# Performance work log

Hardware: AMD Instinct MI355X
Metric: run time of the kernel (lower is better)

## Reference

```python
import jax, jax.numpy as jnp
import numpy as np

N_TOKENS = 16384
IN_FEATURES = 1024
OUT_FEATURES = 1024
BH = 32  # block rows (out dim)
BW = 32  # block cols (in dim)
N_BLOCKS = 256  # density 0.25 * (1024*1024/(32*32))


def setup_inputs() -> dict:
    key = jax.random.key(0)
    k1, k2, k3, k4 = jax.random.split(key, 4)
    x = jax.random.normal(k1, (N_TOKENS, IN_FEATURES), dtype=jnp.float32)
    weight_data = jax.random.normal(k2, (N_BLOCKS, BH, BW), dtype=jnp.float32)
    bias = jnp.zeros((OUT_FEATURES,), dtype=jnp.float32)
    block_row = jax.random.randint(k3, (N_BLOCKS,), 0, OUT_FEATURES // BH, dtype=jnp.int32)
    block_col = jax.random.randint(k4, (N_BLOCKS,), 0, IN_FEATURES // BW, dtype=jnp.int32)
    return {"x": x, "weight_data": weight_data, "bias": bias,
            "block_row": block_row, "block_col": block_col}


def reference(x, weight_data, bias, block_row, block_col):
    # Block-sparse linear: y = x @ W^T + bias, with W[out, in] stored as
    # N_BLOCKS dense (BH, BW) blocks at (block_row, block_col) block coords.
    N = x.shape[0]
    B, bh, bw = weight_data.shape
    n_row_blocks = bias.shape[0] // bh
    x3 = x.reshape(N, -1, bw)           # [N, in/bw, bw]
    xb = x3[:, block_col, :]            # gather input block-columns: [N, B, bw]
    # per-block partial output rows: data[b] @ x_colblock -> [N, B, bh]
    partial = jnp.einsum('nbw,bow->nbo', xb, weight_data)
    y3 = jnp.zeros((N, n_row_blocks, bh), dtype=x.dtype).at[:, block_row, :].add(partial)
    return y3.reshape(N, -1) + bias
```

## Files before the change

kernel.cpp:

```cpp
#include <hip/hip_runtime.h>

#define N_TOKENS 16384
#define IN_F 1024
#define OUT_F 1024
#define NB 256
#define BH 32
#define BW 32
#define NRB 32
#define T_TILE 32
#define XS_STRIDE 1040
#define MAX_SCHED (NB + NRB)
#define SCHED_PAD (MAX_SCHED + 2)
#define WF_SLOT_SHORTS 1024

#define WS_WF_BYTES   (SCHED_PAD * WF_SLOT_SHORTS * 2)
#define WS_SCHED_OFF  WS_WF_BYTES
#define WS_POS_OFF    (WS_SCHED_OFF + SCHED_PAD * 4)
#define WS_WSTART_OFF (WS_POS_OFF + NB * 4)

typedef short short8 __attribute__((ext_vector_type(8)));
typedef float float4v __attribute__((ext_vector_type(4)));

__device__ __forceinline__ short f2bf(float f) {
    unsigned u = __builtin_bit_cast(unsigned, f);
    u += 0x7fffu + ((u >> 16) & 1u);
    return (short)(u >> 16);
}

__global__ void prep_sched_kernel(const int* __restrict__ brow, const int* __restrict__ bcol,
                                  int* __restrict__ sched, int* __restrict__ pos_of,
                                  int* __restrict__ wstart, short* __restrict__ wf)
{
    __shared__ int cnt[NRB], start[NRB], cur[NRB];
    const int tid = threadIdx.x;
    if (tid < NRB) { cnt[tid] = 0; cur[tid] = 0; }
    __syncthreads();
    const int r = brow[tid];
    const int c = bcol[tid];
    atomicAdd(&cnt[r], 1);
    __syncthreads();
    if (tid < NRB) {
        const int w = tid & 3, i = tid >> 2;
        int s = 0;
        for (int rr = 0; rr < NRB; ++rr) {
            const int adj = cnt[rr] > 0 ? cnt[rr] : 1;
            const int ww = rr & 3, ii = rr >> 2;
            if (ww < w || (ww == w && ii < i)) s += adj;
        }
        start[tid] = s;
    }
    if (tid >= 64 && tid < 69) {
        const int w = tid - 64;
        int s = 0;
        for (int rr = 0; rr < NRB; ++rr) {
            const int adj = cnt[rr] > 0 ? cnt[rr] : 1;
            if ((rr & 3) < w) s += adj;
        }
        wstart[w] = s;
    }
    __syncthreads();
    const int slot = atomicAdd(&cur[r], 1);
    const int pos = start[r] + slot;
    sched[pos] = c | (r << 5) | ((slot == cnt[r] - 1) ? (1 << 10) : 0);
    pos_of[tid] = pos;
    if (tid < NRB && cnt[tid] == 0) {
        sched[start[tid]] = (tid << 5) | (1 << 10);
        int4 z = {0, 0, 0, 0};
        int4* dst = (int4*)(wf + (size_t)start[tid] * WF_SLOT_SHORTS);
        for (int q = 0; q < WF_SLOT_SHORTS / 8; ++q) dst[q] = z;
    }
}

__global__ void prep_w_kernel(const float* __restrict__ wd, const int* __restrict__ pos_of,
                              short* __restrict__ wf)
{
    const int g = blockIdx.x * blockDim.x + threadIdx.x;
    const int lane = g & 63;
    const int oh = (g >> 6) & 1;
    const int b = g >> 7;
    const int l16 = lane & 15, quad = lane >> 4;
    const int pos = pos_of[b];
    const float* src = wd + (size_t)b * (BH * BW) + (oh * 16 + l16) * BW + quad * 8;
    const float4 w0 = *(const float4*)src;
    const float4 w1 = *(const float4*)(src + 4);
    short8 o;
    o[0] = f2bf(w0.x); o[1] = f2bf(w0.y); o[2] = f2bf(w0.z); o[3] = f2bf(w0.w);
    o[4] = f2bf(w1.x); o[5] = f2bf(w1.y); o[6] = f2bf(w1.z); o[7] = f2bf(w1.w);
    *(short8*)(wf + (size_t)pos * WF_SLOT_SHORTS + oh * 512 + lane * 8) = o;
}

__global__ __launch_bounds__(256, 2) void spmm_main_kernel(
    const float* __restrict__ x, const float* __restrict__ bias,
    const short* __restrict__ wf, const int* __restrict__ sched_g,
    const int* __restrict__ wstart_g, float* __restrict__ out)
{
    __shared__ short xs[T_TILE * XS_STRIDE];
    __shared__ int ssched[SCHED_PAD];
    __shared__ int swstart[5];

    const int tid = threadIdx.x;
    const int n0 = blockIdx.x * T_TILE;

    {
        const int tr = tid >> 7;
        const int tc = tid & 127;
        const float* xp = x + (size_t)(n0 + tr) * IN_F + tc * 8;
        short* sp = xs + tr * XS_STRIDE + tc * 8;
#pragma unroll
        for (int it = 0; it < T_TILE / 2; ++it) {
            const float4 a = *(const float4*)xp;
            const float4 b = *(const float4*)(xp + 4);
            short8 s;
            s[0] = f2bf(a.x); s[1] = f2bf(a.y); s[2] = f2bf(a.z); s[3] = f2bf(a.w);
            s[4] = f2bf(b.x); s[5] = f2bf(b.y); s[6] = f2bf(b.z); s[7] = f2bf(b.w);
            *(short8*)sp = s;
            xp += 2 * IN_F;
            sp += 2 * XS_STRIDE;
        }
    }
    ssched[tid] = sched_g[tid];
    if (tid < SCHED_PAD - 256) ssched[256 + tid] = sched_g[256 + tid];
    if (tid < 5) swstart[tid] = wstart_g[tid];
    __syncthreads();

    const int lane = tid & 63;
    const int wave = tid >> 6;
    const int l16 = lane & 15, quad = lane >> 4;

    const int s = swstart[wave];
    const int e = swstart[wave + 1];

    const short* x0 = xs + l16 * XS_STRIDE + quad * 8;
    const short* x1 = xs + (16 + l16) * XS_STRIDE + quad * 8;
    const short* wfl = wf + lane * 8;

    int e0 = ssched[s];
    int e1 = ssched[s + 1];
    short8 a0_0 = *(const short8*)(x0 + (e0 & 31) * BW);
    short8 a0_1 = *(const short8*)(x1 + (e0 & 31) * BW);
    short8 wA0 = *(const short8*)(wfl + (size_t)s * WF_SLOT_SHORTS);
    short8 wB0 = *(const short8*)(wfl + (size_t)s * WF_SLOT_SHORTS + 512);
    short8 wA1 = *(const short8*)(wfl + (size_t)(s + 1) * WF_SLOT_SHORTS);
    short8 wB1 = *(const short8*)(wfl + (size_t)(s + 1) * WF_SLOT_SHORTS + 512);

    int rn = wave;
    float bv0 = bias[rn * BH + l16];
    float bv1 = bias[rn * BH + 16 + l16];

    float4v acc00 = {0.f, 0.f, 0.f, 0.f};
    float4v acc01 = {0.f, 0.f, 0.f, 0.f};
    float4v acc10 = {0.f, 0.f, 0.f, 0.f};
    float4v acc11 = {0.f, 0.f, 0.f, 0.f};

    for (int k = s; k < e; ++k) {
        const int ep = ssched[k + 2];
        const short8 wA2 = *(const short8*)(wfl + (size_t)(k + 2) * WF_SLOT_SHORTS);
        const short8 wB2 = *(const short8*)(wfl + (size_t)(k + 2) * WF_SLOT_SHORTS + 512);
        const short8 a1_0 = *(const short8*)(x0 + (e1 & 31) * BW);
        const short8 a1_1 = *(const short8*)(x1 + (e1 & 31) * BW);

        acc00 = __builtin_amdgcn_mfma_f32_16x16x32_bf16(a0_0, wA0, acc00, 0, 0, 0);
        acc01 = __builtin_amdgcn_mfma_f32_16x16x32_bf16(a0_0, wB0, acc01, 0, 0, 0);
        acc10 = __builtin_amdgcn_mfma_f32_16x16x32_bf16(a0_1, wA0, acc10, 0, 0, 0);
        acc11 = __builtin_amdgcn_mfma_f32_16x16x32_bf16(a0_1, wB0, acc11, 0, 0, 0);

        if (e0 & (1 << 10)) {
            const int r = (e0 >> 5) & 31;
            const int ob = r * BH + l16;
            float* op0 = out + (size_t)(n0 + quad * 4) * OUT_F + ob;
            float* op1 = out + (size_t)(n0 + 16 + quad * 4) * OUT_F + ob;
#pragma unroll
            for (int g = 0; g < 4; ++g) {
                op0[g * OUT_F]      = acc00[g] + bv0;
                op0[g * OUT_F + 16] = acc01[g] + bv1;
                op1[g * OUT_F]      = acc10[g] + bv0;
                op1[g * OUT_F + 16] = acc11[g] + bv1;
            }
            acc00 = (float4v){0.f, 0.f, 0.f, 0.f};
            acc01 = (float4v){0.f, 0.f, 0.f, 0.f};
            acc10 = (float4v){0.f, 0.f, 0.f, 0.f};
            acc11 = (float4v){0.f, 0.f, 0.f, 0.f};
            rn = (rn + 4) & 31;
            bv0 = bias[rn * BH + l16];
            bv1 = bias[rn * BH + 16 + l16];
        }
        e0 = e1; e1 = ep;
        a0_0 = a1_0; a0_1 = a1_1;
        wA0 = wA1; wB0 = wB1;
        wA1 = wA2; wB1 = wB2;
    }
}

extern "C" void kernel_launch(void* const* d_in, const int* in_sizes, int n_in,
                              void* d_out, int out_size, void* d_ws, size_t ws_size,
                              hipStream_t stream) {
    const float* x    = (const float*)d_in[0];
    const float* wd   = (const float*)d_in[1];
    const float* bias = (const float*)d_in[2];
    const int* brow   = (const int*)d_in[3];
    const int* bcol   = (const int*)d_in[4];
    float* out = (float*)d_out;

    char* ws = (char*)d_ws;
    short* wf   = (short*)ws;
    int* sched  = (int*)(ws + WS_SCHED_OFF);
    int* pos_of = (int*)(ws + WS_POS_OFF);
    int* wstart = (int*)(ws + WS_WSTART_OFF);

    prep_sched_kernel<<<1, 256, 0, stream>>>(brow, bcol, sched, pos_of, wstart, wf);
    prep_w_kernel<<<NB * 128 / 256, 256, 0, stream>>>(wd, pos_of, wf);
    spmm_main_kernel<<<N_TOKENS / T_TILE, 256, 0, stream>>>(x, bias, wf, sched, wstart, out);
}
```

Measured before the change: 137.4 us.

## Split output row-blocks across eight waves and unroll schedule loop by two

Doubles the block to 512 threads so eight waves each own a quarter as many output row-blocks, and pads each wave's schedule to an even length. The main loop is unrolled by two with weight prefetch four slots ahead and two x-tile fragments loaded per iteration. The aim is shorter per-wave serial chains and more memory-level parallelism on the weight loads. The cost is more registers per thread under a tighter launch bound, plus padding entries with zero weights that may read uninitialized weight slots.

```diff
diff --git a/kernel.cpp b/kernel.cpp
--- a/kernel.cpp
+++ b/kernel.cpp
@@ -8,14 +8,15 @@
 #define BW 32
 #define NRB 32
 #define T_TILE 32
+#define NW 8
 #define XS_STRIDE 1040
-#define MAX_SCHED (NB + NRB)
-#define SCHED_PAD (MAX_SCHED + 2)
+#define SCHED_ALLOC 304
 #define WF_SLOT_SHORTS 1024
-
-#define WS_WF_BYTES   (SCHED_PAD * WF_SLOT_SHORTS * 2)
+#define FLUSH_BIT (1 << 10)
+
+#define WS_WF_BYTES   (SCHED_ALLOC * WF_SLOT_SHORTS * 2)
 #define WS_SCHED_OFF  WS_WF_BYTES
-#define WS_POS_OFF    (WS_SCHED_OFF + SCHED_PAD * 4)
+#define WS_POS_OFF    (WS_SCHED_OFF + SCHED_ALLOC * 4)
 #define WS_WSTART_OFF (WS_POS_OFF + NB * 4)
 
 typedef short short8 __attribute__((ext_vector_type(8)));
@@ -40,31 +41,54 @@
     atomicAdd(&cnt[r], 1);
     __syncthreads();
     if (tid < NRB) {
-        const int w = tid & 3, i = tid >> 2;
+        const int w = tid & 7;
         int s = 0;
-        for (int rr = 0; rr < NRB; ++rr) {
-            const int adj = cnt[rr] > 0 ? cnt[rr] : 1;
-            const int ww = rr & 3, ii = rr >> 2;
-            if (ww < w || (ww == w && ii < i)) s += adj;
-        }
+        for (int w2 = 0; w2 < w; ++w2) {
+            int t = 0;
+            for (int rr = w2; rr < NRB; rr += NW) t += (cnt[rr] ? cnt[rr] : 1);
+            s += (t + 1) & ~1;
+        }
+        for (int rr = w; rr < tid; rr += NW) s += (cnt[rr] ? cnt[rr] : 1);
         start[tid] = s;
     }
-    if (tid >= 64 && tid < 69) {
+    if (tid >= 64 && tid < 64 + NW + 1) {
         const int w = tid - 64;
         int s = 0;
-        for (int rr = 0; rr < NRB; ++rr) {
-            const int adj = cnt[rr] > 0 ? cnt[rr] : 1;
-            if ((rr & 3) < w) s += adj;
+        for (int w2 = 0; w2 < w; ++w2) {
+            int t = 0;
+            for (int rr = w2; rr < NRB; rr += NW) t += (cnt[rr] ? cnt[rr] : 1);
+            s += (t + 1) & ~1;
         }
         wstart[w] = s;
+    }
+    if (tid >= 96 && tid < 96 + NW) {
+        const int w = tid - 96;
+        int base = 0;
+        for (int w2 = 0; w2 < w; ++w2) {
+            int t = 0;
+            for (int rr = w2; rr < NRB; rr += NW) t += (cnt[rr] ? cnt[rr] : 1);
+            base += (t + 1) & ~1;
+        }
+        int t = 0;
+        for (int rr = w; rr < NRB; rr += NW) t += (cnt[rr] ? cnt[rr] : 1);
+        if (t & 1) sched[base + t] = 0;
+    }
+    if (tid >= 128 && tid < 136) {
+        int tot = 0;
+        for (int w2 = 0; w2 < NW; ++w2) {
+            int t = 0;
+            for (int rr = w2; rr < NRB; rr += NW) t += (cnt[rr] ? cnt[rr] : 1);
+            tot += (t + 1) & ~1;
+        }
+        sched[tot + (tid - 128)] = 0;
     }
     __syncthreads();
     const int slot = atomicAdd(&cur[r], 1);
     const int pos = start[r] + slot;
-    sched[pos] = c | (r << 5) | ((slot == cnt[r] - 1) ? (1 << 10) : 0);
+    sched[pos] = c | (r << 5) | ((slot == cnt[r] - 1) ? FLUSH_BIT : 0);
     pos_of[tid] = pos;
     if (tid < NRB && cnt[tid] == 0) {
-        sched[start[tid]] = (tid << 5) | (1 << 10);
+        sched[start[tid]] = (tid << 5) | FLUSH_BIT;
         int4 z = {0, 0, 0, 0};
         int4* dst = (int4*)(wf + (size_t)start[tid] * WF_SLOT_SHORTS);
         for (int q = 0; q < WF_SLOT_SHORTS / 8; ++q) dst[q] = z;
@@ -89,14 +113,14 @@
     *(short8*)(wf + (size_t)pos * WF_SLOT_SHORTS + oh * 512 + lane * 8) = o;
 }
 
-__global__ __launch_bounds__(256, 2) void spmm_main_kernel(
+__global__ __launch_bounds__(512, 4) void spmm_main_kernel(
     const float* __restrict__ x, const float* __restrict__ bias,
     const short* __restrict__ wf, const int* __restrict__ sched_g,
     const int* __restrict__ wstart_g, float* __restrict__ out)
 {
     __shared__ short xs[T_TILE * XS_STRIDE];
-    __shared__ int ssched[SCHED_PAD];
-    __shared__ int swstart[5];
+    __shared__ int ssched[SCHED_ALLOC];
+    __shared__ int swstart[NW + 1];
 
     const int tid = threadIdx.x;
     const int n0 = blockIdx.x * T_TILE;
@@ -107,20 +131,19 @@
         const float* xp = x + (size_t)(n0 + tr) * IN_F + tc * 8;
         short* sp = xs + tr * XS_STRIDE + tc * 8;
 #pragma unroll
-        for (int it = 0; it < T_TILE / 2; ++it) {
+        for (int it = 0; it < T_TILE / 4; ++it) {
             const float4 a = *(const float4*)xp;
             const float4 b = *(const float4*)(xp + 4);
             short8 s;
             s[0] = f2bf(a.x); s[1] = f2bf(a.y); s[2] = f2bf(a.z); s[3] = f2bf(a.w);
             s[4] = f2bf(b.x); s[5] = f2bf(b.y); s[6] = f2bf(b.z); s[7] = f2bf(b.w);
             *(short8*)sp = s;
-            xp += 2 * IN_F;
-            sp += 2 * XS_STRIDE;
-        }
-    }
-    ssched[tid] = sched_g[tid];
-    if (tid < SCHED_PAD - 256) ssched[256 + tid] = sched_g[256 + tid];
-    if (tid < 5) swstart[tid] = wstart_g[tid];
+            xp += 4 * IN_F;
+            sp += 4 * XS_STRIDE;
+        }
+    }
+    if (tid < SCHED_ALLOC) ssched[tid] = sched_g[tid];
+    if (tid < NW + 1) swstart[tid] = wstart_g[tid];
     __syncthreads();
 
     const int lane = tid & 63;
@@ -131,63 +154,83 @@
     const int e = swstart[wave + 1];
 
     const short* x0 = xs + l16 * XS_STRIDE + quad * 8;
-    const short* x1 = xs + (16 + l16) * XS_STRIDE + quad * 8;
+    const short* x1 = x0 + 16 * XS_STRIDE;
     const short* wfl = wf + lane * 8;
 
-    int e0 = ssched[s];
-    int e1 = ssched[s + 1];
-    short8 a0_0 = *(const short8*)(x0 + (e0 & 31) * BW);
-    short8 a0_1 = *(const short8*)(x1 + (e0 & 31) * BW);
-    short8 wA0 = *(const short8*)(wfl + (size_t)s * WF_SLOT_SHORTS);
-    short8 wB0 = *(const short8*)(wfl + (size_t)s * WF_SLOT_SHORTS + 512);
-    short8 wA1 = *(const short8*)(wfl + (size_t)(s + 1) * WF_SLOT_SHORTS);
-    short8 wB1 = *(const short8*)(wfl + (size_t)(s + 1) * WF_SLOT_SHORTS + 512);
+    int e0 = ssched[s], e1 = ssched[s + 1];
+    int e2 = ssched[s + 2], e3 = ssched[s + 3];
+    short8 cwA0 = *(const short8*)(wfl + (size_t)s * WF_SLOT_SHORTS);
+    short8 cwB0 = *(const short8*)(wfl + (size_t)s * WF_SLOT_SHORTS + 512);
+    short8 cwA1 = *(const short8*)(wfl + (size_t)(s + 1) * WF_SLOT_SHORTS);
+    short8 cwB1 = *(const short8*)(wfl + (size_t)(s + 1) * WF_SLOT_SHORTS + 512);
+    short8 nwA0 = *(const short8*)(wfl + (size_t)(s + 2) * WF_SLOT_SHORTS);
+    short8 nwB0 = *(const short8*)(wfl + (size_t)(s + 2) * WF_SLOT_SHORTS + 512);
+    short8 nwA1 = *(const short8*)(wfl + (size_t)(s + 3) * WF_SLOT_SHORTS);
+    short8 nwB1 = *(const short8*)(wfl + (size_t)(s + 3) * WF_SLOT_SHORTS + 512);
+    short8 a0t0 = *(const short8*)(x0 + (e0 & 31) * BW);
+    short8 a0t1 = *(const short8*)(x1 + (e0 & 31) * BW);
+    short8 a1t0 = *(const short8*)(x0 + (e1 & 31) * BW);
+    short8 a1t1 = *(const short8*)(x1 + (e1 & 31) * BW);
 
     int rn = wave;
     float bv0 = bias[rn * BH + l16];
     float bv1 = bias[rn * BH + 16 + l16];
 
-    float4v acc00 = {0.f, 0.f, 0.f, 0.f};
-    float4v acc01 = {0.f, 0.f, 0.f, 0.f};
-    float4v acc10 = {0.f, 0.f, 0.f, 0.f};
-    float4v acc11 = {0.f, 0.f, 0.f, 0.f};
-
-    for (int k = s; k < e; ++k) {
-        const int ep = ssched[k + 2];
-        const short8 wA2 = *(const short8*)(wfl + (size_t)(k + 2) * WF_SLOT_SHORTS);
-        const short8 wB2 = *(const short8*)(wfl + (size_t)(k + 2) * WF_SLOT_SHORTS + 512);
-        const short8 a1_0 = *(const short8*)(x0 + (e1 & 31) * BW);
-        const short8 a1_1 = *(const short8*)(x1 + (e1 & 31) * BW);
-
-        acc00 = __builtin_amdgcn_mfma_f32_16x16x32_bf16(a0_0, wA0, acc00, 0, 0, 0);
-        acc01 = __builtin_amdgcn_mfma_f32_16x16x32_bf16(a0_0, wB0, acc01, 0, 0, 0);
-        acc10 = __builtin_amdgcn_mfma_f32_16x16x32_bf16(a0_1, wA0, acc10, 0, 0, 0);
-        acc11 = __builtin_amdgcn_mfma_f32_16x16x32_bf16(a0_1, wB0, acc11, 0, 0, 0);
-
-        if (e0 & (1 << 10)) {
-            const int r = (e0 >> 5) & 31;
-            const int ob = r * BH + l16;
+    float4v accA = {0.f, 0.f, 0.f, 0.f};
+    float4v accB = {0.f, 0.f, 0.f, 0.f};
+    float4v accC = {0.f, 0.f, 0.f, 0.f};
+    float4v accD = {0.f, 0.f, 0.f, 0.f};
+
+    auto flush = [&](int ev) {
+        if (ev & FLUSH_BIT) {
+            const int rr = (ev >> 5) & 31;
+            const int ob = rr * BH + l16;
             float* op0 = out + (size_t)(n0 + quad * 4) * OUT_F + ob;
-            float* op1 = out + (size_t)(n0 + 16 + quad * 4) * OUT_F + ob;
+            float* op1 = op0 + (size_t)16 * OUT_F;
 #pragma unroll
             for (int g = 0; g < 4; ++g) {
-                op0[g * OUT_F]      = acc00[g] + bv0;
-                op0[g * OUT_F + 16] = acc01[g] + bv1;
-                op1[g * OUT_F]      = acc10[g] + bv0;
-                op1[g * OUT_F + 16] = acc11[g] + bv1;
+                op0[g * OUT_F]      = accA[g] + bv0;
+                op0[g * OUT_F + 16] = accB[g] + bv1;
+                op1[g * OUT_F]      = accC[g] + bv0;
+                op1[g * OUT_F + 16] = accD[g] + bv1;
             }
-            acc00 = (float4v){0.f, 0.f, 0.f, 0.f};
-            acc01 = (float4v){0.f, 0.f, 0.f, 0.f};
-            acc10 = (float4v){0.f, 0.f, 0.f, 0.f};
-            acc11 = (float4v){0.f, 0.f, 0.f, 0.f};
-            rn = (rn + 4) & 31;
+            accA = (float4v){0.f, 0.f, 0.f, 0.f};
+            accB = (float4v){0.f, 0.f, 0.f, 0.f};
+            accC = (float4v){0.f, 0.f, 0.f, 0.f};
+            accD = (float4v){0.f, 0.f, 0.f, 0.f};
+            rn = (rn + NW) & 31;
             bv0 = bias[rn * BH + l16];
             bv1 = bias[rn * BH + 16 + l16];
         }
-        e0 = e1; e1 = ep;
-        a0_0 = a1_0; a0_1 = a1_1;
-        wA0 = wA1; wB0 = wB1;
-        wA1 = wA2; wB1 = wB2;
+    };
+
+    for (int k = s; k < e; k += 2) {
+        const int e4 = ssched[k + 4];
+        const int e5 = ssched[k + 5];
+        const short8 fwA0 = *(const short8*)(wfl + (size_t)(k + 4) * WF_SLOT_SHORTS);
+        const short8 fwB0 = *(const short8*)(wfl + (size_t)(k + 4) * WF_SLOT_SHORTS + 512);
+        const short8 fwA1 = *(const short8*)(wfl + (size_t)(k + 5) * WF_SLOT_SHORTS);
+        const short8 fwB1 = *(const short8*)(wfl + (size_t)(k + 5) * WF_SLOT_SHORTS + 512);
+        const short8 na0t0 = *(const short8*)(x0 + (e2 & 31) * BW);
+        const short8 na0t1 = *(const short8*)(x1 + (e2 & 31) * BW);
+        const short8 na1t0 = *(const short8*)(x0 + (e3 & 31) * BW);
+        const short8 na1t1 = *(const short8*)(x1 + (e3 & 31) * BW);
+
+        accA = __builtin_amdgcn_mfma_f32_16x16x32_bf16(a0t0, cwA0, accA, 0, 0, 0);
+        accB = __builtin_amdgcn_mfma_f32_16x16x32_bf16(a0t0, cwB0, accB, 0, 0, 0);
+        accC = __builtin_amdgcn_mfma_f32_16x16x32_bf16(a0t1, cwA0, accC, 0, 0, 0);
+        accD = __builtin_amdgcn_mfma_f32_16x16x32_bf16(a0t1, cwB0, accD, 0, 0, 0);
+        flush(e0);
+        accA = __builtin_amdgcn_mfma_f32_16x16x32_bf16(a1t0, cwA1, accA, 0, 0, 0);
+        accB = __builtin_amdgcn_mfma_f32_16x16x32_bf16(a1t0, cwB1, accB, 0, 0, 0);
+        accC = __builtin_amdgcn_mfma_f32_16x16x32_bf16(a1t1, cwA1, accC, 0, 0, 0);
+        accD = __builtin_amdgcn_mfma_f32_16x16x32_bf16(a1t1, cwB1, accD, 0, 0, 0);
+        flush(e1);
+
+        e0 = e2; e1 = e3; e2 = e4; e3 = e5;
+        a0t0 = na0t0; a0t1 = na0t1; a1t0 = na1t0; a1t1 = na1t1;
+        cwA0 = nwA0; cwB0 = nwB0; cwA1 = nwA1; cwB1 = nwB1;
+        nwA0 = fwA0; nwB0 = fwB0; nwA1 = fwA1; nwB1 = fwB1;
     }
 }
 
@@ -209,5 +252,5 @@
 
     prep_sched_kernel<<<1, 256, 0, stream>>>(brow, bcol, sched, pos_of, wstart, wf);
     prep_w_kernel<<<NB * 128 / 256, 256, 0, stream>>>(wd, pos_of, wf);
-    spmm_main_kernel<<<N_TOKENS / T_TILE, 256, 0, stream>>>(x, bias, wf, sched, wstart, out);
-}
+    spmm_main_kernel<<<N_TOKENS / T_TILE, 512, 0, stream>>>(x, bias, wf, sched, wstart, out);
+}
```

Measured after the change: 133.6 us. 2.8% less time.

## Balance row buckets across 16 waves and switch to 32x32x16 MFMA with 64-token tiles

Applied to the files above, without the earlier changes.

The schedule now sorts output row-blocks by block count and pairs the heaviest with the lightest into 16 buckets, one per wave of a 1024-thread workgroup. The workgroup covers 64 tokens instead of 32. The inner loop uses 32x32x16 bf16 MFMA with a weight layout rewritten to match, and the weight prefetch depth drops from two to one. The goal is to even out per-wave work (the old code split rows round-robin across 4 waves) and to reuse each staged x tile across more output rows. In exchange the kernel uses more LDS per workgroup (~133KB), which may limit occupancy, and the serial single-thread sort adds prep cost.

```diff
diff --git a/kernel.cpp b/kernel.cpp
--- a/kernel.cpp
+++ b/kernel.cpp
@@ -7,19 +7,21 @@
 #define BH 32
 #define BW 32
 #define NRB 32
-#define T_TILE 32
+#define T_TILE 64
+#define NWAVES 16
+#define NBUCKET 16
 #define XS_STRIDE 1040
-#define MAX_SCHED (NB + NRB)
-#define SCHED_PAD (MAX_SCHED + 2)
+#define SCHED_ALLOC 304
 #define WF_SLOT_SHORTS 1024
-
-#define WS_WF_BYTES   (SCHED_PAD * WF_SLOT_SHORTS * 2)
+#define FLUSH_BIT (1 << 10)
+
+#define WS_WF_BYTES   (SCHED_ALLOC * WF_SLOT_SHORTS * 2)
 #define WS_SCHED_OFF  WS_WF_BYTES
-#define WS_POS_OFF    (WS_SCHED_OFF + SCHED_PAD * 4)
+#define WS_POS_OFF    (WS_SCHED_OFF + SCHED_ALLOC * 4)
 #define WS_WSTART_OFF (WS_POS_OFF + NB * 4)
 
 typedef short short8 __attribute__((ext_vector_type(8)));
-typedef float float4v __attribute__((ext_vector_type(4)));
+typedef float float16v __attribute__((ext_vector_type(16)));
 
 __device__ __forceinline__ short f2bf(float f) {
     unsigned u = __builtin_bit_cast(unsigned, f);
@@ -31,42 +33,44 @@
                                   int* __restrict__ sched, int* __restrict__ pos_of,
                                   int* __restrict__ wstart, short* __restrict__ wf)
 {
-    __shared__ int cnt[NRB], start[NRB], cur[NRB];
+    __shared__ int cnt[NRB], rstart[NRB];
+    __shared__ short srow[NB];
     const int tid = threadIdx.x;
-    if (tid < NRB) { cnt[tid] = 0; cur[tid] = 0; }
+    if (tid < NRB) cnt[tid] = 0;
     __syncthreads();
     const int r = brow[tid];
     const int c = bcol[tid];
+    srow[tid] = (short)r;
     atomicAdd(&cnt[r], 1);
     __syncthreads();
-    if (tid < NRB) {
-        const int w = tid & 3, i = tid >> 2;
-        int s = 0;
-        for (int rr = 0; rr < NRB; ++rr) {
-            const int adj = cnt[rr] > 0 ? cnt[rr] : 1;
-            const int ww = rr & 3, ii = rr >> 2;
-            if (ww < w || (ww == w && ii < i)) s += adj;
-        }
-        start[tid] = s;
-    }
-    if (tid >= 64 && tid < 69) {
-        const int w = tid - 64;
-        int s = 0;
-        for (int rr = 0; rr < NRB; ++rr) {
-            const int adj = cnt[rr] > 0 ? cnt[rr] : 1;
-            if ((rr & 3) < w) s += adj;
-        }
-        wstart[w] = s;
-    }
-    __syncthreads();
-    const int slot = atomicAdd(&cur[r], 1);
-    const int pos = start[r] + slot;
-    sched[pos] = c | (r << 5) | ((slot == cnt[r] - 1) ? (1 << 10) : 0);
+    if (tid == 0) {
+        int adj[NRB], ord[NRB];
+        for (int i = 0; i < NRB; ++i) { adj[i] = cnt[i] ? cnt[i] : 1; ord[i] = i; }
+        for (int i = 0; i < NRB - 1; ++i) {
+            int m = i;
+            for (int j = i + 1; j < NRB; ++j) if (adj[ord[j]] > adj[ord[m]]) m = j;
+            const int t = ord[i]; ord[i] = ord[m]; ord[m] = t;
+        }
+        int pos = 0;
+        for (int b = 0; b < NBUCKET; ++b) {
+            wstart[b] = pos;
+            const int r1 = ord[b], r2 = ord[31 - b];
+            rstart[r1] = pos; pos += adj[r1];
+            rstart[r2] = pos; pos += adj[r2];
+        }
+        wstart[NBUCKET] = pos;
+        sched[pos] = 0; sched[pos + 1] = 0;
+    }
+    __syncthreads();
+    int slot = 0;
+    for (int b2 = 0; b2 < tid; ++b2) slot += (srow[b2] == r);
+    const int pos = rstart[r] + slot;
+    sched[pos] = c | (r << 5) | ((slot == cnt[r] - 1) ? FLUSH_BIT : 0);
     pos_of[tid] = pos;
     if (tid < NRB && cnt[tid] == 0) {
-        sched[start[tid]] = (tid << 5) | (1 << 10);
+        sched[rstart[tid]] = (tid << 5) | FLUSH_BIT;
         int4 z = {0, 0, 0, 0};
-        int4* dst = (int4*)(wf + (size_t)start[tid] * WF_SLOT_SHORTS);
+        int4* dst = (int4*)(wf + (size_t)rstart[tid] * WF_SLOT_SHORTS);
         for (int q = 0; q < WF_SLOT_SHORTS / 8; ++q) dst[q] = z;
     }
 }
@@ -76,27 +80,26 @@
 {
     const int g = blockIdx.x * blockDim.x + threadIdx.x;
     const int lane = g & 63;
-    const int oh = (g >> 6) & 1;
+    const int h = (g >> 6) & 1;
     const int b = g >> 7;
-    const int l16 = lane & 15, quad = lane >> 4;
     const int pos = pos_of[b];
-    const float* src = wd + (size_t)b * (BH * BW) + (oh * 16 + l16) * BW + quad * 8;
+    const float* src = wd + (size_t)b * (BH * BW) + (lane & 31) * BW + h * 16 + (lane >> 5) * 8;
     const float4 w0 = *(const float4*)src;
     const float4 w1 = *(const float4*)(src + 4);
     short8 o;
     o[0] = f2bf(w0.x); o[1] = f2bf(w0.y); o[2] = f2bf(w0.z); o[3] = f2bf(w0.w);
     o[4] = f2bf(w1.x); o[5] = f2bf(w1.y); o[6] = f2bf(w1.z); o[7] = f2bf(w1.w);
-    *(short8*)(wf + (size_t)pos * WF_SLOT_SHORTS + oh * 512 + lane * 8) = o;
-}
-
-__global__ __launch_bounds__(256, 2) void spmm_main_kernel(
+    *(short8*)(wf + (size_t)pos * WF_SLOT_SHORTS + h * 512 + lane * 8) = o;
+}
+
+__global__ __launch_bounds__(1024, 4) void spmm_main_kernel(
     const float* __restrict__ x, const float* __restrict__ bias,
     const short* __restrict__ wf, const int* __restrict__ sched_g,
     const int* __restrict__ wstart_g, float* __restrict__ out)
 {
     __shared__ short xs[T_TILE * XS_STRIDE];
-    __shared__ int ssched[SCHED_PAD];
-    __shared__ int swstart[5];
+    __shared__ int ssched[SCHED_ALLOC];
+    __shared__ int swstart[NBUCKET + 1];
 
     const int tid = threadIdx.x;
     const int n0 = blockIdx.x * T_TILE;
@@ -107,87 +110,82 @@
         const float* xp = x + (size_t)(n0 + tr) * IN_F + tc * 8;
         short* sp = xs + tr * XS_STRIDE + tc * 8;
 #pragma unroll
-        for (int it = 0; it < T_TILE / 2; ++it) {
+        for (int it = 0; it < T_TILE / 8; ++it) {
             const float4 a = *(const float4*)xp;
             const float4 b = *(const float4*)(xp + 4);
             short8 s;
             s[0] = f2bf(a.x); s[1] = f2bf(a.y); s[2] = f2bf(a.z); s[3] = f2bf(a.w);
             s[4] = f2bf(b.x); s[5] = f2bf(b.y); s[6] = f2bf(b.z); s[7] = f2bf(b.w);
             *(short8*)sp = s;
-            xp += 2 * IN_F;
-            sp += 2 * XS_STRIDE;
-        }
-    }
-    ssched[tid] = sched_g[tid];
-    if (tid < SCHED_PAD - 256) ssched[256 + tid] = sched_g[256 + tid];
-    if (tid < 5) swstart[tid] = wstart_g[tid];
+            xp += 8 * IN_F;
+            sp += 8 * XS_STRIDE;
+        }
+    }
+    if (tid < SCHED_ALLOC) ssched[tid] = sched_g[tid];
+    if (tid < NBUCKET + 1) swstart[tid] = wstart_g[tid];
     __syncthreads();
 
     const int lane = tid & 63;
     const int wave = tid >> 6;
-    const int l16 = lane & 15, quad = lane >> 4;
+    const int l32 = lane & 31;
+    const int kg = lane >> 5;
 
     const int s = swstart[wave];
     const int e = swstart[wave + 1];
 
-    const short* x0 = xs + l16 * XS_STRIDE + quad * 8;
-    const short* x1 = xs + (16 + l16) * XS_STRIDE + quad * 8;
+    const short* xA = xs + l32 * XS_STRIDE + kg * 8;
     const short* wfl = wf + lane * 8;
 
     int e0 = ssched[s];
     int e1 = ssched[s + 1];
-    short8 a0_0 = *(const short8*)(x0 + (e0 & 31) * BW);
-    short8 a0_1 = *(const short8*)(x1 + (e0 & 31) * BW);
-    short8 wA0 = *(const short8*)(wfl + (size_t)s * WF_SLOT_SHORTS);
-    short8 wB0 = *(const short8*)(wfl + (size_t)s * WF_SLOT_SHORTS + 512);
-    short8 wA1 = *(const short8*)(wfl + (size_t)(s + 1) * WF_SLOT_SHORTS);
-    short8 wB1 = *(const short8*)(wfl + (size_t)(s + 1) * WF_SLOT_SHORTS + 512);
-
-    int rn = wave;
-    float bv0 = bias[rn * BH + l16];
-    float bv1 = bias[rn * BH + 16 + l16];
-
-    float4v acc00 = {0.f, 0.f, 0.f, 0.f};
-    float4v acc01 = {0.f, 0.f, 0.f, 0.f};
-    float4v acc10 = {0.f, 0.f, 0.f, 0.f};
-    float4v acc11 = {0.f, 0.f, 0.f, 0.f};
+    {
+    }
+    const int c0 = (e0 & 31) * BW;
+    short8 wh0 = *(const short8*)(wfl + (size_t)s * WF_SLOT_SHORTS);
+    short8 wh1 = *(const short8*)(wfl + (size_t)s * WF_SLOT_SHORTS + 512);
+    short8 a00 = *(const short8*)(xA + c0);
+    short8 a01 = *(const short8*)(xA + c0 + 16);
+    short8 a10 = *(const short8*)(xA + 32 * XS_STRIDE + c0);
+    short8 a11 = *(const short8*)(xA + 32 * XS_STRIDE + c0 + 16);
+
+    float bv = bias[((e0 >> 5) & 31) * BH + l32];
+
+    const float16v zero16 = {0.f,0.f,0.f,0.f, 0.f,0.f,0.f,0.f, 0.f,0.f,0.f,0.f, 0.f,0.f,0.f,0.f};
+    float16v acc0 = zero16;
+    float16v acc1 = zero16;
 
     for (int k = s; k < e; ++k) {
-        const int ep = ssched[k + 2];
-        const short8 wA2 = *(const short8*)(wfl + (size_t)(k + 2) * WF_SLOT_SHORTS);
-        const short8 wB2 = *(const short8*)(wfl + (size_t)(k + 2) * WF_SLOT_SHORTS + 512);
-        const short8 a1_0 = *(const short8*)(x0 + (e1 & 31) * BW);
-        const short8 a1_1 = *(const short8*)(x1 + (e1 & 31) * BW);
-
-        acc00 = __builtin_amdgcn_mfma_f32_16x16x32_bf16(a0_0, wA0, acc00, 0, 0, 0);
-        acc01 = __builtin_amdgcn_mfma_f32_16x16x32_bf16(a0_0, wB0, acc01, 0, 0, 0);
-        acc10 = __builtin_amdgcn_mfma_f32_16x16x32_bf16(a0_1, wA0, acc10, 0, 0, 0);
-        acc11 = __builtin_amdgcn_mfma_f32_16x16x32_bf16(a0_1, wB0, acc11, 0, 0, 0);
-
-        if (e0 & (1 << 10)) {
-            const int r = (e0 >> 5) & 31;
-            const int ob = r * BH + l16;
-            float* op0 = out + (size_t)(n0 + quad * 4) * OUT_F + ob;
-            float* op1 = out + (size_t)(n0 + 16 + quad * 4) * OUT_F + ob;
+        const int en = ssched[k + 2];
+        const int cn = (e1 & 31) * BW;
+        const short8 nwh0 = *(const short8*)(wfl + (size_t)(k + 1) * WF_SLOT_SHORTS);
+        const short8 nwh1 = *(const short8*)(wfl + (size_t)(k + 1) * WF_SLOT_SHORTS + 512);
+        const short8 na00 = *(const short8*)(xA + cn);
+        const short8 na01 = *(const short8*)(xA + cn + 16);
+        const short8 na10 = *(const short8*)(xA + 32 * XS_STRIDE + cn);
+        const short8 na11 = *(const short8*)(xA + 32 * XS_STRIDE + cn + 16);
+
+        acc0 = __builtin_amdgcn_mfma_f32_32x32x16_bf16(a00, wh0, acc0, 0, 0, 0);
+        acc0 = __builtin_amdgcn_mfma_f32_32x32x16_bf16(a01, wh1, acc0, 0, 0, 0);
+        acc1 = __builtin_amdgcn_mfma_f32_32x32x16_bf16(a10, wh0, acc1, 0, 0, 0);
+        acc1 = __builtin_amdgcn_mfma_f32_32x32x16_bf16(a11, wh1, acc1, 0, 0, 0);
+
+        if (e0 & FLUSH_BIT) {
+            const int rr = (e0 >> 5) & 31;
+            const int ob = rr * BH + l32;
+            float* op0 = out + (size_t)n0 * OUT_F + ob;
 #pragma unroll
-            for (int g = 0; g < 4; ++g) {
-                op0[g * OUT_F]      = acc00[g] + bv0;
-                op0[g * OUT_F + 16] = acc01[g] + bv1;
-                op1[g * OUT_F]      = acc10[g] + bv0;
-                op1[g * OUT_F + 16] = acc11[g] + bv1;
+            for (int reg = 0; reg < 16; ++reg) {
+                const int row = (reg & 3) + 8 * (reg >> 2) + 4 * kg;
+                op0[(size_t)row * OUT_F] = acc0[reg] + bv;
+                op0[(size_t)(row + 32) * OUT_F] = acc1[reg] + bv;
             }
-            acc00 = (float4v){0.f, 0.f, 0.f, 0.f};
-            acc01 = (float4v){0.f, 0.f, 0.f, 0.f};
-            acc10 = (float4v){0.f, 0.f, 0.f, 0.f};
-            acc11 = (float4v){0.f, 0.f, 0.f, 0.f};
-            rn = (rn + 4) & 31;
-            bv0 = bias[rn * BH + l16];
-            bv1 = bias[rn * BH + 16 + l16];
-        }
-        e0 = e1; e1 = ep;
-        a0_0 = a1_0; a0_1 = a1_1;
-        wA0 = wA1; wB0 = wB1;
-        wA1 = wA2; wB1 = wB2;
+            acc0 = zero16;
+            acc1 = zero16;
+            bv = bias[((e1 >> 5) & 31) * BH + l32];
+        }
+        e0 = e1; e1 = en;
+        a00 = na00; a01 = na01; a10 = na10; a11 = na11;
+        wh0 = nwh0; wh1 = nwh1;
     }
 }
 
@@ -209,5 +207,5 @@
 
     prep_sched_kernel<<<1, 256, 0, stream>>>(brow, bcol, sched, pos_of, wstart, wf);
     prep_w_kernel<<<NB * 128 / 256, 256, 0, stream>>>(wd, pos_of, wf);
-    spmm_main_kernel<<<N_TOKENS / T_TILE, 256, 0, stream>>>(x, bias, wf, sched, wstart, out);
-}
+    spmm_main_kernel<<<N_TOKENS / T_TILE, 1024, 0, stream>>>(x, bias, wf, sched, wstart, out);
+}
```

Result: slower. 194.7 us (+41.7%).
